# Kernel optimization log

Hardware: AMD Instinct MI355X
Metric: run time of the kernel (lower is better)

The kernel has to match this reference:

```python
import jax, jax.numpy as jnp
import numpy as np

EMBED_DIM = 1024
NUM_HEADS = 16
HEAD_DIM = EMBED_DIM // NUM_HEADS


def setup_inputs() -> dict:
    key = jax.random.key(0)
    ks = jax.random.split(key, 11)
    B, S, E = 4, 2048, EMBED_DIM
    s = 1.0 / np.sqrt(E)
    return {
        "query": jax.random.normal(ks[0], (B, S, E), jnp.float32),
        "key": jax.random.normal(ks[1], (B, S, E), jnp.float32),
        "value": jax.random.normal(ks[2], (B, S, E), jnp.float32),
        "Wq": jax.random.normal(ks[3], (E, E), jnp.float32) * s,
        "bq": jnp.zeros((E,), jnp.float32),
        "Wk": jax.random.normal(ks[4], (E, E), jnp.float32) * s,
        "bk": jnp.zeros((E,), jnp.float32),
        "Wv": jax.random.normal(ks[5], (E, E), jnp.float32) * s,
        "bv": jnp.zeros((E,), jnp.float32),
        "Wo": jax.random.normal(ks[6], (E, E), jnp.float32) * s,
        "bo": jnp.zeros((E,), jnp.float32),
    }


def reference(query, key, value, Wq, bq, Wk, bk, Wv, bv, Wo, bo):
    B, S, E = query.shape
    H, D = NUM_HEADS, HEAD_DIM
    scale = jnp.float32(np.sqrt(D))
    # linear projections (torch Linear: x @ W.T + b)
    Q = (query @ Wq.T + bq).reshape(B, S, H, D).transpose(0, 2, 1, 3)  # [B,H,S,D]
    K = (key @ Wk.T + bk).reshape(B, S, H, D).transpose(0, 2, 1, 3)
    V = (value @ Wv.T + bv).reshape(B, S, H, D).transpose(0, 2, 1, 3)
    # full O(S^2) score materialization, matching the eager torch code
    scores = jnp.einsum("bhqd,bhkd->bhqk", Q, K) / scale  # [B,H,S,S]
    attn = jax.nn.softmax(scores, axis=-1)
    out = jnp.einsum("bhqk,bhkd->bhqd", attn, V)  # [B,H,S,D]
    out = out.transpose(0, 2, 1, 3).reshape(B, S, E)
    out = out @ Wo.T + bo
    return out, attn.mean(axis=1)
```

## Files before the change

### kernel.cpp

```cpp
#include <hip/hip_runtime.h>
#include <hip/hip_bf16.h>

#define DEVI __device__ __forceinline__

typedef __bf16 bf16x8 __attribute__((ext_vector_type(8)));
typedef __bf16 bf16x4 __attribute__((ext_vector_type(4)));
typedef float f32x4 __attribute__((ext_vector_type(4)));

constexpr int B_ = 4, S_ = 2048, E_ = 1024, H_ = 16, D_ = 64;
constexpr int N_ = B_ * S_;
constexpr float SC2_ = 0.18033688011112042f;

constexpr size_t XB_OFF = 0;
constexpr size_t WB_OFF = 50331648;
constexpr size_t QB_OFF = 58720256;
constexpr size_t KB_OFF = 75497472;
constexpr size_t VT_OFF = 92274688;
constexpr size_t CTX_OFF = 109051904;
constexpr size_t LS_OFF = 125829120;
constexpr size_t WS_NEED = 126353408;

typedef const __attribute__((address_space(1))) void* gas_ptr;
typedef __attribute__((address_space(3))) void* las_ptr;

DEVI void load_lds16(const void* g, void* l) {
  __builtin_amdgcn_global_load_lds((gas_ptr)g, (las_ptr)l, 16, 0, 0);
}

DEVI f32x4 mfma16(bf16x8 a, bf16x8 b, f32x4 c) {
  return __builtin_amdgcn_mfma_f32_16x16x32_bf16(a, b, c, 0, 0, 0);
}

DEVI int swz(int row) { return ((row >> 1) ^ (row >> 3)) & 3; }

#if __has_builtin(__builtin_amdgcn_exp2f)
DEVI float ex2(float x) { return __builtin_amdgcn_exp2f(x); }
#else
DEVI float ex2(float x) { return exp2f(x); }
#endif

__global__ __launch_bounds__(256) void conv_x(const float* __restrict__ q,
                                              const float* __restrict__ k,
                                              const float* __restrict__ v,
                                              __bf16* __restrict__ dst) {
  const float* src = (blockIdx.y == 0) ? q : ((blockIdx.y == 1) ? k : v);
  __bf16* d = dst + (size_t)blockIdx.y * N_ * E_;
  size_t i = ((size_t)blockIdx.x * blockDim.x + threadIdx.x) * 4;
  float4 f = *(const float4*)(src + i);
  bf16x4 o;
  o[0] = (__bf16)f.x; o[1] = (__bf16)f.y; o[2] = (__bf16)f.z; o[3] = (__bf16)f.w;
  *(bf16x4*)(d + i) = o;
}

__global__ __launch_bounds__(256) void conv_w(const float* __restrict__ wq,
                                              const float* __restrict__ wk,
                                              const float* __restrict__ wv,
                                              const float* __restrict__ wo,
                                              __bf16* __restrict__ dst) {
  const float* src = (blockIdx.y == 0) ? wq : ((blockIdx.y == 1) ? wk :
                     ((blockIdx.y == 2) ? wv : wo));
  __bf16* d = dst + (size_t)blockIdx.y * E_ * E_;
  size_t i = ((size_t)blockIdx.x * blockDim.x + threadIdx.x) * 4;
  float4 f = *(const float4*)(src + i);
  bf16x4 o;
  o[0] = (__bf16)f.x; o[1] = (__bf16)f.y; o[2] = (__bf16)f.z; o[3] = (__bf16)f.w;
  *(bf16x4*)(d + i) = o;
}

__global__ __launch_bounds__(256) void gemm_qkv(const __bf16* __restrict__ Xb,
                                                const __bf16* __restrict__ Wb,
                                                const float* __restrict__ bq,
                                                const float* __restrict__ bk,
                                                const float* __restrict__ bv,
                                                __bf16* __restrict__ Qb,
                                                __bf16* __restrict__ Kb,
                                                __bf16* __restrict__ Vt) {
  __shared__ __attribute__((aligned(16))) __bf16 As[128 * 32];
  __shared__ __attribute__((aligned(16))) __bf16 Bs[128 * 32];
  const int z = blockIdx.z;
  const __bf16* A = Xb + (size_t)z * N_ * E_;
  const __bf16* W = Wb + (size_t)z * E_ * E_;
  const float* bias = (z == 0) ? bq : ((z == 1) ? bk : bv);
  const int m0 = blockIdx.x * 128, n0 = blockIdx.y * 128;
  const int t = threadIdx.x, lane = t & 63, w = t >> 6;
  const int wm = w >> 1, wn = w & 1;
  const int l15 = lane & 15, g = lane >> 4;

  f32x4 acc[4][4] = {};

  for (int kk = 0; kk < E_; kk += 32) {
#pragma unroll
    for (int i = 0; i < 2; ++i) {
      int c = t + i * 256;
      int row = c >> 2, kc = c & 3;
      int sl = kc ^ swz(row);
      load_lds16(A + (size_t)(m0 + row) * E_ + kk + sl * 8, (void*)(As + c * 8));
      load_lds16(W + (size_t)(n0 + row) * E_ + kk + sl * 8, (void*)(Bs + c * 8));
    }
    __syncthreads();
    bf16x8 a[4], b[4];
#pragma unroll
    for (int i = 0; i < 4; ++i) {
      int row = wm * 64 + i * 16 + l15;
      a[i] = *(const bf16x8*)(As + row * 32 + (g ^ swz(row)) * 8);
    }
#pragma unroll
    for (int j = 0; j < 4; ++j) {
      int row = wn * 64 + j * 16 + l15;
      b[j] = *(const bf16x8*)(Bs + row * 32 + (g ^ swz(row)) * 8);
    }
#pragma unroll
    for (int i = 0; i < 4; ++i)
#pragma unroll
      for (int j = 0; j < 4; ++j)
        acc[i][j] = mfma16(a[i], b[j], acc[i][j]);
    __syncthreads();
  }

#pragma unroll
  for (int i = 0; i < 4; ++i) {
    int mloc = wm * 64 + i * 16 + (g << 2);
#pragma unroll
    for (int j = 0; j < 4; ++j) {
      int nloc = wn * 64 + j * 16 + l15;
      int n = n0 + nloc;
      int h = n >> 6, d = n & 63;
      float bs = bias[n];
      if (z == 2) {
        int m = m0 + mloc;
        int bb = m >> 11, s = m & 2047;
        bf16x4 pk;
#pragma unroll
        for (int r = 0; r < 4; ++r) pk[r] = (__bf16)(acc[i][j][r] + bs);
        *(bf16x4*)(Vt + ((size_t)(bb * H_ + h) * D_ + d) * S_ + s) = pk;
      } else {
        __bf16* dst = (z == 0) ? Qb : Kb;
#pragma unroll
        for (int r = 0; r < 4; ++r) {
          int m = m0 + mloc + r;
          int bb = m >> 11, s = m & 2047;
          dst[((size_t)(bb * H_ + h) * S_ + s) * D_ + d] = (__bf16)(acc[i][j][r] + bs);
        }
      }
    }
  }
}

__global__ __launch_bounds__(256, 4) void attn_pv(const __bf16* __restrict__ Qb,
                                                  const __bf16* __restrict__ Kb,
                                                  const __bf16* __restrict__ Vt,
                                                  float* __restrict__ Lsum,
                                                  __bf16* __restrict__ Ctx) {
  __shared__ __attribute__((aligned(16))) __bf16 smem[2][8192];

  const int q0 = blockIdx.x * 128;
  const int bh = blockIdx.y;
  const __bf16* Qh = Qb + (size_t)bh * S_ * D_;
  const __bf16* Kh = Kb + (size_t)bh * S_ * D_;
  const __bf16* Vh = Vt + (size_t)bh * D_ * S_;
  const int t = threadIdx.x, lane = t & 63, w = t >> 6;
  const int l15 = lane & 15, g = lane >> 4;
  const int ksel = 8 * (l15 >> 2) + (l15 & 3);

  bf16x8 qf[2][2];
#pragma unroll
  for (int jb = 0; jb < 2; ++jb) {
    int row = w * 32 + jb * 16 + l15;
#pragma unroll
    for (int ks = 0; ks < 2; ++ks)
      qf[jb][ks] = *(const bf16x8*)(Qh + (size_t)(q0 + row) * D_ + ks * 32 + g * 8);
  }

  bf16x8 ones;
#pragma unroll
  for (int i = 0; i < 8; ++i) ones[i] = (__bf16)1.0f;

  f32x4 acc[4][2] = {};
  f32x4 lacc[2] = {};

  auto stage_kv = [&](int kk0, __bf16* buf) {
#pragma unroll
    for (int i = 0; i < 2; ++i) {
      int c = t + i * 256;
      int sub = c >> 8, rem = c & 255, row = rem >> 2, kc = rem & 3;
      int sl = kc ^ swz(row);
      load_lds16(Kh + (size_t)(kk0 + row) * D_ + sub * 32 + sl * 8, (void*)(buf + c * 8));
      load_lds16(Vh + (size_t)row * S_ + kk0 + sub * 32 + sl * 8, (void*)(buf + 4096 + c * 8));
    }
  };

  auto compute = [&](const __bf16* Ksb) {
    const __bf16* Vsb = Ksb + 4096;
#pragma unroll
    for (int chunk = 0; chunk < 2; ++chunk) {
      f32x4 sc[2][2];
#pragma unroll
      for (int blk = 0; blk < 2; ++blk) {
        int krow = chunk * 32 + 4 * blk + ksel;
        int so = (g ^ swz(krow)) * 8;
        bf16x8 kf0 = *(const bf16x8*)(Ksb + krow * 32 + so);
        bf16x8 kf1 = *(const bf16x8*)(Ksb + 2048 + krow * 32 + so);
#pragma unroll
        for (int jb = 0; jb < 2; ++jb) {
          f32x4 s = {};
          s = mfma16(kf0, qf[jb][0], s);
          s = mfma16(kf1, qf[jb][1], s);
          sc[blk][jb] = s;
        }
      }
      bf16x8 pf[2];
#pragma unroll
      for (int jb = 0; jb < 2; ++jb) {
#pragma unroll
        for (int r = 0; r < 4; ++r) {
          pf[jb][r]     = (__bf16)ex2(sc[0][jb][r] * SC2_);
          pf[jb][4 + r] = (__bf16)ex2(sc[1][jb][r] * SC2_);
        }
        lacc[jb] = mfma16(ones, pf[jb], lacc[jb]);
      }
      __builtin_amdgcn_s_setprio(1);
#pragma unroll
      for (int mb = 0; mb < 4; ++mb) {
        int row = mb * 16 + l15;
        bf16x8 vf = *(const bf16x8*)(Vsb + chunk * 2048 + row * 32 + (g ^ swz(row)) * 8);
#pragma unroll
        for (int jb = 0; jb < 2; ++jb)
          acc[mb][jb] = mfma16(vf, pf[jb], acc[mb][jb]);
      }
      __builtin_amdgcn_s_setprio(0);
    }
  };

  stage_kv(0, smem[0]);
  stage_kv(64, smem[1]);

  for (int tt = 0; tt < 30; ++tt) {
    asm volatile("s_waitcnt vmcnt(4)" ::: "memory");
    __builtin_amdgcn_s_barrier();
    compute(smem[tt & 1]);
    __builtin_amdgcn_s_barrier();
    stage_kv((tt + 2) * 64, smem[tt & 1]);
  }
  asm volatile("s_waitcnt vmcnt(4)" ::: "memory");
  __builtin_amdgcn_s_barrier();
  compute(smem[0]);
  asm volatile("s_waitcnt vmcnt(0)" ::: "memory");
  __builtin_amdgcn_s_barrier();
  compute(smem[1]);

  if (lane < 16) {
#pragma unroll
    for (int jb = 0; jb < 2; ++jb)
      Lsum[(size_t)bh * S_ + q0 + w * 32 + jb * 16 + lane] = lacc[jb][0];
  }

  const int bb = bh >> 4, h = bh & 15;
#pragma unroll
  for (int jb = 0; jb < 2; ++jb) {
    float invl = 1.0f / lacc[jb][0];
    int q = q0 + w * 32 + jb * 16 + l15;
#pragma unroll
    for (int mb = 0; mb < 4; ++mb) {
      int d = mb * 16 + (g << 2);
      bf16x4 pk;
#pragma unroll
      for (int r = 0; r < 4; ++r) pk[r] = (__bf16)(acc[mb][jb][r] * invl);
      *(bf16x4*)(Ctx + ((size_t)bb * S_ + q) * E_ + h * 64 + d) = pk;
    }
  }
}


DEVI void attn_mean_body(int id, __bf16* smem,
                         const __bf16* __restrict__ Qb,
                         const __bf16* __restrict__ Kb,
                         const float* __restrict__ Lsum,
                         float* __restrict__ meanout) {
  __bf16* Qs  = smem;
  __bf16* Ks2 = smem + 8192;
  const int k0 = (id & 15) * 128;
  const int q0 = ((id >> 4) & 15) * 128;
  const int bI = id >> 8;
  const int t = threadIdx.x, lane = t & 63, w = t >> 6;
  const int l15 = lane & 15, g = lane >> 4;
  const int ksel = 8 * (l15 >> 2) + (l15 & 3);

  f32x4 macc[4][2][2] = {};

  for (int h = 0; h < H_; ++h) {
    const size_t bh = (size_t)bI * H_ + h;
    const __bf16* Qh = Qb + bh * S_ * D_;
    const __bf16* Kh = Kb + bh * S_ * D_;
#pragma unroll
    for (int i = 0; i < 4; ++i) {
      int c = t + i * 256;
      int sub = c >> 9, rem = c & 511, row = rem >> 2, kc = rem & 3;
      int sl = kc ^ swz(row);
      load_lds16(Qh + (size_t)(q0 + row) * D_ + sub * 32 + sl * 8, (void*)(Qs + c * 8));
      load_lds16(Kh + (size_t)(k0 + row) * D_ + sub * 32 + sl * 8, (void*)(Ks2 + c * 8));
    }
    float invl[2];
#pragma unroll
    for (int jb = 0; jb < 2; ++jb)
      invl[jb] = 1.0f / Lsum[bh * S_ + q0 + w * 32 + jb * 16 + l15];
    __syncthreads();

    bf16x8 qf[2][2];
#pragma unroll
    for (int jb = 0; jb < 2; ++jb) {
      int row = w * 32 + jb * 16 + l15;
#pragma unroll
      for (int ks = 0; ks < 2; ++ks)
        qf[jb][ks] = *(const bf16x8*)(Qs + ks * 4096 + row * 32 + (g ^ swz(row)) * 8);
    }

#pragma unroll
    for (int chunk = 0; chunk < 4; ++chunk) {
#pragma unroll
      for (int blk = 0; blk < 2; ++blk) {
        int krow = chunk * 32 + 4 * blk + ksel;
        int so = (g ^ swz(krow)) * 8;
        bf16x8 kf0 = *(const bf16x8*)(Ks2 + krow * 32 + so);
        bf16x8 kf1 = *(const bf16x8*)(Ks2 + 4096 + krow * 32 + so);
#pragma unroll
        for (int jb = 0; jb < 2; ++jb) {
          f32x4 s = {};
          s = mfma16(kf0, qf[jb][0], s);
          s = mfma16(kf1, qf[jb][1], s);
#pragma unroll
          for (int r = 0; r < 4; ++r)
            macc[chunk][blk][jb][r] += ex2(s[r] * SC2_) * invl[jb];
        }
      }
    }
    __syncthreads();
  }

#pragma unroll
  for (int chunk = 0; chunk < 4; ++chunk)
#pragma unroll
    for (int blk = 0; blk < 2; ++blk)
#pragma unroll
      for (int jb = 0; jb < 2; ++jb) {
        int q = q0 + w * 32 + jb * 16 + l15;
        int kb = k0 + chunk * 32 + 8 * g + 4 * blk;
        f32x4 o;
#pragma unroll
        for (int r = 0; r < 4; ++r) o[r] = macc[chunk][blk][jb][r] * 0.0625f;
        *(f32x4*)(meanout + ((size_t)bI * S_ + q) * S_ + kb) = o;
      }
}

DEVI void gemm_out_body(int id, __bf16* smem,
                        const __bf16* __restrict__ Ctx,
                        const __bf16* __restrict__ Wo,
                        const float* __restrict__ bo,
                        float* __restrict__ out) {
  __bf16* As = smem;
  __bf16* Bs = smem + 4096;
  const int m0 = (id & 63) * 128, n0 = (id >> 6) * 128;
  const int t = threadIdx.x, lane = t & 63, w = t >> 6;
  const int wm = w >> 1, wn = w & 1;
  const int l15 = lane & 15, g = lane >> 4;

  f32x4 acc[4][4] = {};

  for (int kk = 0; kk < E_; kk += 32) {
#pragma unroll
    for (int i = 0; i < 2; ++i) {
      int c = t + i * 256;
      int row = c >> 2, kc = c & 3;
      int sl = kc ^ swz(row);
      load_lds16(Ctx + (size_t)(m0 + row) * E_ + kk + sl * 8, (void*)(As + c * 8));
      load_lds16(Wo + (size_t)(n0 + row) * E_ + kk + sl * 8, (void*)(Bs + c * 8));
    }
    __syncthreads();
    bf16x8 a[4], b[4];
#pragma unroll
    for (int i = 0; i < 4; ++i) {
      int row = wm * 64 + i * 16 + l15;
      a[i] = *(const bf16x8*)(As + row * 32 + (g ^ swz(row)) * 8);
    }
#pragma unroll
    for (int j = 0; j < 4; ++j) {
      int row = wn * 64 + j * 16 + l15;
      b[j] = *(const bf16x8*)(Bs + row * 32 + (g ^ swz(row)) * 8);
    }
#pragma unroll
    for (int i = 0; i < 4; ++i)
#pragma unroll
      for (int j = 0; j < 4; ++j)
        acc[i][j] = mfma16(a[i], b[j], acc[i][j]);
    __syncthreads();
  }

#pragma unroll
  for (int i = 0; i < 4; ++i) {
    int mloc = wm * 64 + i * 16 + (g << 2);
#pragma unroll
    for (int j = 0; j < 4; ++j) {
      int n = n0 + wn * 64 + j * 16 + l15;
      float bs = bo[n];
#pragma unroll
      for (int r = 0; r < 4; ++r)
        out[(size_t)(m0 + mloc + r) * E_ + n] = acc[i][j][r] + bs;
    }
  }
}

__global__ __launch_bounds__(256, 3) void tail_fused(const __bf16* __restrict__ Qb,
                                                     const __bf16* __restrict__ Kb,
                                                     const float* __restrict__ Lsum,
                                                     float* __restrict__ meanout,
                                                     const __bf16* __restrict__ Ctx,
                                                     const __bf16* __restrict__ Wo,
                                                     const float* __restrict__ bo,
                                                     float* __restrict__ out) {
  __shared__ __attribute__((aligned(16))) __bf16 smem[16384];
  const int bid = blockIdx.x;
  const int g3 = bid / 3, r3 = bid - g3 * 3;
  if (r3 == 2)
    gemm_out_body(g3, smem, Ctx, Wo, bo, out);
  else
    attn_mean_body(2 * g3 + r3, smem, Qb, Kb, Lsum, meanout);
}

extern "C" void kernel_launch(void* const* d_in, const int* in_sizes, int n_in,
                              void* d_out, int out_size, void* d_ws, size_t ws_size,
                              hipStream_t stream) {
  if (ws_size < WS_NEED) {
    hipMemsetAsync(d_out, 0, (size_t)out_size * sizeof(float), stream);
    return;
  }

  const float* q  = (const float*)d_in[0];
  const float* k  = (const float*)d_in[1];
  const float* v  = (const float*)d_in[2];
  const float* Wq = (const float*)d_in[3];
  const float* bq = (const float*)d_in[4];
  const float* Wk = (const float*)d_in[5];
  const float* bk = (const float*)d_in[6];
  const float* Wv = (const float*)d_in[7];
  const float* bv = (const float*)d_in[8];
  const float* Wo = (const float*)d_in[9];
  const float* bo = (const float*)d_in[10];

  char* ws = (char*)d_ws;
  __bf16* Xb  = (__bf16*)(ws + XB_OFF);
  __bf16* Wb  = (__bf16*)(ws + WB_OFF);
  __bf16* Qb  = (__bf16*)(ws + QB_OFF);
  __bf16* Kb  = (__bf16*)(ws + KB_OFF);
  __bf16* Vt  = (__bf16*)(ws + VT_OFF);
  __bf16* Ctx = (__bf16*)(ws + CTX_OFF);
  float*  Ls  = (float*)(ws + LS_OFF);

  float* out0 = (float*)d_out;
  float* out1 = (float*)d_out + (size_t)N_ * E_;

  conv_x<<<dim3(N_ * E_ / 4 / 256, 3), 256, 0, stream>>>(q, k, v, Xb);
  conv_w<<<dim3(E_ * E_ / 4 / 256, 4), 256, 0, stream>>>(Wq, Wk, Wv, Wo, Wb);
  gemm_qkv<<<dim3(N_ / 128, E_ / 128, 3), 256, 0, stream>>>(Xb, Wb, bq, bk, bv, Qb, Kb, Vt);
  attn_pv<<<dim3(S_ / 128, B_ * H_), 256, 0, stream>>>(Qb, Kb, Vt, Ls, Ctx);
  tail_fused<<<dim3(1536), 256, 0, stream>>>(Qb, Kb, Ls, out1, Ctx,
                                             Wb + 3 * (size_t)E_ * E_, bo, out0);
}
```

Before: 430.0 us.

## Double-buffer K tiles across heads in attention-mean and load Q directly

The per-head loop in the attention-mean body now prefetches the next head's K tile into a second LDS buffer while the current head is computed, so each iteration needs one barrier instead of two. Q fragments are read straight from global memory into registers rather than staged through LDS. The head loop is fully unrolled and the launch-bounds occupancy hint is raised from 3 to 4 blocks per CU. The intent is to hide global-load latency behind the MFMA and exp work, at the risk of register pressure or spills from the tighter occupancy target and the unrolled loop.

```diff
diff --git a/kernel.cpp b/kernel.cpp
--- a/kernel.cpp
+++ b/kernel.cpp
@@ -276,8 +276,6 @@
                          const __bf16* __restrict__ Kb,
                          const float* __restrict__ Lsum,
                          float* __restrict__ meanout) {
-  __bf16* Qs  = smem;
-  __bf16* Ks2 = smem + 8192;
   const int k0 = (id & 15) * 128;
   const int q0 = ((id >> 4) & 15) * 128;
   const int bI = id >> 8;
@@ -285,34 +283,50 @@
   const int l15 = lane & 15, g = lane >> 4;
   const int ksel = 8 * (l15 >> 2) + (l15 & 3);
 
+  const __bf16* Qbase = Qb + (size_t)bI * H_ * S_ * D_;
+  const __bf16* Kbase = Kb + (size_t)bI * H_ * S_ * D_;
+  const float* Lbase = Lsum + (size_t)bI * H_ * S_;
+
   f32x4 macc[4][2][2] = {};
 
-  for (int h = 0; h < H_; ++h) {
-    const size_t bh = (size_t)bI * H_ + h;
-    const __bf16* Qh = Qb + bh * S_ * D_;
-    const __bf16* Kh = Kb + bh * S_ * D_;
+  auto stage_k = [&](int h, __bf16* buf) {
+    const __bf16* Kh = Kbase + (size_t)h * S_ * D_;
 #pragma unroll
     for (int i = 0; i < 4; ++i) {
       int c = t + i * 256;
       int sub = c >> 9, rem = c & 511, row = rem >> 2, kc = rem & 3;
       int sl = kc ^ swz(row);
-      load_lds16(Qh + (size_t)(q0 + row) * D_ + sub * 32 + sl * 8, (void*)(Qs + c * 8));
-      load_lds16(Kh + (size_t)(k0 + row) * D_ + sub * 32 + sl * 8, (void*)(Ks2 + c * 8));
+      load_lds16(Kh + (size_t)(k0 + row) * D_ + sub * 32 + sl * 8, (void*)(buf + c * 8));
+    }
+  };
+
+  stage_k(0, smem);
+
+#pragma unroll
+  for (int h = 0; h < H_; ++h) {
+    __bf16* cur = (h & 1) ? (smem + 8192) : smem;
+    __bf16* nxt = (h & 1) ? smem : (smem + 8192);
+
+    asm volatile("s_waitcnt vmcnt(0)" ::: "memory");
+    __builtin_amdgcn_s_barrier();
+
+    const __bf16* Qh = Qbase + (size_t)h * S_ * D_;
+    bf16x8 qf[2][2];
+#pragma unroll
+    for (int jb = 0; jb < 2; ++jb) {
+      int row = q0 + w * 32 + jb * 16 + l15;
+#pragma unroll
+      for (int ks = 0; ks < 2; ++ks)
+        qf[jb][ks] = *(const bf16x8*)(Qh + (size_t)row * D_ + ks * 32 + g * 8);
     }
     float invl[2];
 #pragma unroll
     for (int jb = 0; jb < 2; ++jb)
-      invl[jb] = 1.0f / Lsum[bh * S_ + q0 + w * 32 + jb * 16 + l15];
-    __syncthreads();
-
-    bf16x8 qf[2][2];
-#pragma unroll
-    for (int jb = 0; jb < 2; ++jb) {
-      int row = w * 32 + jb * 16 + l15;
-#pragma unroll
-      for (int ks = 0; ks < 2; ++ks)
-        qf[jb][ks] = *(const bf16x8*)(Qs + ks * 4096 + row * 32 + (g ^ swz(row)) * 8);
-    }
+      invl[jb] = 1.0f / Lbase[(size_t)h * S_ + q0 + w * 32 + jb * 16 + l15];
+
+    __builtin_amdgcn_sched_barrier(0);
+    if (h + 1 < H_) stage_k(h + 1, nxt);
+    __builtin_amdgcn_sched_barrier(0);
 
 #pragma unroll
     for (int chunk = 0; chunk < 4; ++chunk) {
@@ -320,8 +334,8 @@
       for (int blk = 0; blk < 2; ++blk) {
         int krow = chunk * 32 + 4 * blk + ksel;
         int so = (g ^ swz(krow)) * 8;
-        bf16x8 kf0 = *(const bf16x8*)(Ks2 + krow * 32 + so);
-        bf16x8 kf1 = *(const bf16x8*)(Ks2 + 4096 + krow * 32 + so);
+        bf16x8 kf0 = *(const bf16x8*)(cur + krow * 32 + so);
+        bf16x8 kf1 = *(const bf16x8*)(cur + 4096 + krow * 32 + so);
 #pragma unroll
         for (int jb = 0; jb < 2; ++jb) {
           f32x4 s = {};
@@ -333,7 +347,6 @@
         }
       }
     }
-    __syncthreads();
   }
 
 #pragma unroll
@@ -408,7 +421,7 @@
   }
 }
 
-__global__ __launch_bounds__(256, 3) void tail_fused(const __bf16* __restrict__ Qb,
+__global__ __launch_bounds__(256, 4) void tail_fused(const __bf16* __restrict__ Qb,
                                                      const __bf16* __restrict__ Kb,
                                                      const float* __restrict__ Lsum,
                                                      float* __restrict__ meanout,
```

Measured after the change: 1.103 ms. 2.57x slower.
